# Kernel optimization log

Measured on AMD Instinct MI355X. Metric: run time of the kernel, lower is better.

Reference implementation:

```python
import jax, jax.numpy as jnp
import numpy as np

EPS = 1e-5  # torch LayerNorm default

def _ln(x, g, b):
    m = jnp.mean(x, axis=-1, keepdims=True)
    v = jnp.var(x, axis=-1, keepdims=True)
    return (x - m) / jnp.sqrt(v + EPS) * g + b

def setup_inputs() -> dict:
    B, S, F, H = 32, 512, 32, 128
    key = jax.random.key(0)
    ks = jax.random.split(key, 20)
    sc = 0.05
    inp = {
        "x": jax.random.normal(ks[0], (B, S, F), dtype=jnp.float32),
        # per-feature GRNs, stacked along F. fc1: Linear(1,H) -> weight vec (F,H)
        "fw1": jax.random.normal(ks[1], (F, H), dtype=jnp.float32) * sc,
        "fb1": jax.random.normal(ks[2], (F, H), dtype=jnp.float32) * sc,
        "fw2": jax.random.normal(ks[3], (F, H, H), dtype=jnp.float32) * sc,
        "fb2": jax.random.normal(ks[4], (F, H), dtype=jnp.float32) * sc,
        "fglu_w": jax.random.normal(ks[5], (F, H, 2 * H), dtype=jnp.float32) * sc,
        "fglu_b": jax.random.normal(ks[6], (F, 2 * H), dtype=jnp.float32) * sc,
        "fskip": jax.random.normal(ks[7], (F, H), dtype=jnp.float32) * sc,  # skip_proj Linear(1,H,bias=False)
        "fln_g": jnp.ones((F, H), dtype=jnp.float32),
        "fln_b": jnp.zeros((F, H), dtype=jnp.float32),
        # weight GRN: Linear(F,H)->ELU->Linear(H,F)->GLU(F)->LN(F); skip is identity (F==F)
        "ww1": jax.random.normal(ks[8], (F, H), dtype=jnp.float32) * sc,
        "wb1": jax.random.normal(ks[9], (H,), dtype=jnp.float32) * sc,
        "ww2": jax.random.normal(ks[10], (H, F), dtype=jnp.float32) * sc,
        "wb2": jax.random.normal(ks[11], (F,), dtype=jnp.float32) * sc,
        "wglu_w": jax.random.normal(ks[12], (F, 2 * F), dtype=jnp.float32) * sc,
        "wglu_b": jax.random.normal(ks[13], (2 * F,), dtype=jnp.float32) * sc,
        "wln_g": jnp.ones((F,), dtype=jnp.float32),
        "wln_b": jnp.zeros((F,), dtype=jnp.float32),
    }
    return inp

def reference(x, fw1, fb1, fw2, fb2, fglu_w, fglu_b, fskip, fln_g, fln_b,
              ww1, wb1, ww2, wb2, wglu_w, wglu_b, wln_g, wln_b):
    # ---- per-feature GRNs, batched over the F axis (dropout = eval, identity) ----
    # fc1(Linear(1,H)) + ELU : x[...,f] is a scalar per token
    h = jax.nn.elu(x[..., None] * fw1 + fb1)                 # (B,S,F,H)
    h = jnp.einsum('bsfh,fho->bsfo', h, fw2) + fb2           # fc2 (B,S,F,H)
    g = jnp.einsum('bsfh,fho->bsfo', h, fglu_w) + fglu_b     # GLU pre-act (B,S,F,2H)
    v, gate = jnp.split(g, 2, axis=-1)
    glu = v * jax.nn.sigmoid(gate)                           # (B,S,F,H)
    skip = x[..., None] * fskip                              # skip_proj (B,S,F,H)
    processed = _ln(glu + skip, fln_g[None, None], fln_b[None, None])  # (B,S,F,H)

    # ---- weight GRN over the full feature vector ----
    wh = jax.nn.elu(jnp.einsum('bsf,fh->bsh', x, ww1) + wb1)  # (B,S,H)
    wh = jnp.einsum('bsh,hf->bsf', wh, ww2) + wb2             # (B,S,F)
    wg = jnp.einsum('bsf,fg->bsg', wh, wglu_w) + wglu_b       # (B,S,2F)
    wv, wgate = jnp.split(wg, 2, axis=-1)
    wglu = wv * jax.nn.sigmoid(wgate)
    w = _ln(wglu + x, wln_g, wln_b)                           # skip is identity (F==F)
    weights = jax.nn.softmax(w, axis=-1)                      # (B,S,F)

    out = jnp.einsum('bsf,bsfh->bsh', weights, processed)     # weighted combine
    return (out, weights)
```

## Files before the change

kernel.cpp:

```cpp
#include <hip/hip_runtime.h>
#include <cstdint>
#include <cstddef>

#define NTOK 16384
#define FDIM 32
#define HDIM 128
#define TOKB 32

typedef __attribute__((ext_vector_type(8))) short short8;
typedef __attribute__((ext_vector_type(4))) float float4v;
typedef __attribute__((ext_vector_type(2))) float float2v;
typedef __attribute__((ext_vector_type(4))) unsigned int uint4v;

__device__ __forceinline__ float elu_f(float x)  { return x > 0.f ? x : __expf(x) - 1.f; }
__device__ __forceinline__ float sigm_f(float x) { return 1.f / (1.f + __expf(-x)); }

__device__ __forceinline__ unsigned int f2bf(float f) {
  unsigned int u = __float_as_uint(f);
  u += 0x7FFFu + ((u >> 16) & 1u);
  return u >> 16;
}
__device__ __forceinline__ unsigned int cvtpk(float lo, float hi) {
  unsigned int r;
  asm("v_cvt_pk_bf16_f32 %0, %1, %2" : "=v"(r) : "v"(lo), "v"(hi));
  return r;
}

__global__ __launch_bounds__(256) void k_pw(
    const float* __restrict__ x,
    const float* __restrict__ fw2, const float* __restrict__ fb2,
    const float* __restrict__ fglu_w, const float* __restrict__ fglu_b,
    const float* __restrict__ ww1, const float* __restrict__ wb1,
    const float* __restrict__ ww2, const float* __restrict__ wb2,
    const float* __restrict__ wglu_w, const float* __restrict__ wglu_b,
    const float* __restrict__ wln_g, const float* __restrict__ wln_b,
    unsigned short* __restrict__ bfrag, float* __restrict__ bcomb,
    float* __restrict__ wout)
{
  __shared__ __align__(16) float smem[4096];
  const int tid = threadIdx.x;

  if (blockIdx.x < 128) {
    const int f  = blockIdx.x >> 2;
    const int ks = blockIdx.x & 3;
    const float* src = fw2 + ((size_t)f * 128 + ks * 32) * 128;
    for (int i = 0; i < 4; ++i) {
      int vi = tid + i * 256;
      *(float4v*)&smem[vi * 4] = *(const float4v*)&src[vi * 4];
    }
    __syncthreads();

    const int o2 = tid;
    float acc[32];
#pragma unroll
    for (int kk = 0; kk < 32; ++kk) acc[kk] = 0.f;
    float bacc = 0.f;

    for (int o = 0; o < 128; o += 4) {
      float gv0 = fglu_w[((size_t)f * 128 + o + 0) * 256 + o2];
      float gv1 = fglu_w[((size_t)f * 128 + o + 1) * 256 + o2];
      float gv2 = fglu_w[((size_t)f * 128 + o + 2) * 256 + o2];
      float gv3 = fglu_w[((size_t)f * 128 + o + 3) * 256 + o2];
      bacc += fb2[f * 128 + o + 0] * gv0 + fb2[f * 128 + o + 1] * gv1
            + fb2[f * 128 + o + 2] * gv2 + fb2[f * 128 + o + 3] * gv3;
#pragma unroll
      for (int kk = 0; kk < 32; ++kk) {
        float4v a4 = *(const float4v*)&smem[kk * 128 + o];
        acc[kk] += a4[0] * gv0 + a4[1] * gv1 + a4[2] * gv2 + a4[3] * gv3;
      }
    }

    const int type = o2 >> 7;
    const int h    = o2 & 127;
    const int w2   = h >> 4;
    const int r    = h & 15;
    const size_t tbase = ((((size_t)f * 8 + w2) * 2 + type) * 4 + ks) * 512;
#pragma unroll
    for (int gg = 0; gg < 4; ++gg) {
      uint4v pk;
      pk[0] = f2bf(acc[gg * 8 + 0]) | (f2bf(acc[gg * 8 + 1]) << 16);
      pk[1] = f2bf(acc[gg * 8 + 2]) | (f2bf(acc[gg * 8 + 3]) << 16);
      pk[2] = f2bf(acc[gg * 8 + 4]) | (f2bf(acc[gg * 8 + 5]) << 16);
      pk[3] = f2bf(acc[gg * 8 + 6]) | (f2bf(acc[gg * 8 + 7]) << 16);
      *(uint4v*)(bfrag + tbase + (size_t)(r + gg * 16) * 8) = pk;
    }
    if (ks == 0)
      bcomb[f * 256 + o2] = bacc + fglu_b[f * 256 + o2];

  } else {
    const int bid = blockIdx.x - 128;
    const int wv  = tid >> 6;
    const int l   = tid & 63;
    const int t   = bid * 4 + wv;
    float* S = smem + wv * 256;

    float xv = x[(size_t)t * 32 + (l & 31)];
    if (l < 32) S[l] = xv;
    float a0 = wb1[l], a1 = wb1[l + 64];
    __syncthreads();
    for (int f2 = 0; f2 < 32; ++f2) {
      float xf = S[f2];
      a0 = fmaf(xf, ww1[f2 * 128 + l], a0);
      a1 = fmaf(xf, ww1[f2 * 128 + l + 64], a1);
    }
    a0 = elu_f(a0); a1 = elu_f(a1);
    S[32 + l] = a0; S[32 + l + 64] = a1;
    __syncthreads();

    const int o    = l & 31;
    const int half = l >> 5;
    float b = 0.f;
    for (int hh = 0; hh < 64; ++hh)
      b = fmaf(S[32 + half * 64 + hh], ww2[(half * 64 + hh) * 32 + o], b);
    b += __shfl_xor(b, 32);
    b += wb2[o];
    S[160 + o] = b;
    __syncthreads();

    float g = wglu_b[l];
    for (int o2i = 0; o2i < 32; ++o2i)
      g = fmaf(S[160 + o2i], wglu_w[o2i * 64 + l], g);

    float gate = __shfl_xor(g, 32);
    float y = g * sigm_f(gate) + xv;
    float s = y;
    s += __shfl_xor(s, 1); s += __shfl_xor(s, 2); s += __shfl_xor(s, 4);
    s += __shfl_xor(s, 8); s += __shfl_xor(s, 16);
    float mean = s * (1.f / 32.f);
    float d = y - mean;
    float ss = d * d;
    ss += __shfl_xor(ss, 1); ss += __shfl_xor(ss, 2); ss += __shfl_xor(ss, 4);
    ss += __shfl_xor(ss, 8); ss += __shfl_xor(ss, 16);
    float rstd = rsqrtf(ss * (1.f / 32.f) + 1e-5f);
    const int cc = l & 31;
    float ln = d * rstd * wln_g[cc] + wln_b[cc];
    float mx = ln;
    mx = fmaxf(mx, __shfl_xor(mx, 1));  mx = fmaxf(mx, __shfl_xor(mx, 2));
    mx = fmaxf(mx, __shfl_xor(mx, 4));  mx = fmaxf(mx, __shfl_xor(mx, 8));
    mx = fmaxf(mx, __shfl_xor(mx, 16));
    float e = __expf(ln - mx);
    float se = e;
    se += __shfl_xor(se, 1); se += __shfl_xor(se, 2); se += __shfl_xor(se, 4);
    se += __shfl_xor(se, 8); se += __shfl_xor(se, 16);
    if (l < 32) wout[(size_t)t * 32 + l] = e / se;
  }
}

__global__ __launch_bounds__(512, 4) void k_main(
    const float* __restrict__ x,
    const float* __restrict__ fw1, const float* __restrict__ fb1,
    const float* __restrict__ fskip, const float* __restrict__ flng,
    const float* __restrict__ flnb,
    const unsigned short* __restrict__ bfrag, const float* __restrict__ bcomb,
    const float* __restrict__ wts, float* __restrict__ out)
{
  __shared__ __align__(16) unsigned short a_lds[TOKB * 128];
  __shared__ __align__(16) float x_lds[FDIM * TOKB];
  __shared__ __align__(16) float w_lds[FDIM * TOKB];
  __shared__ __align__(16) float sred[2][2][TOKB];

  const int tid = threadIdx.x;
  const int w   = tid >> 6;
  const int l   = tid & 63;
  const int tk  = l & 15;
  const int rg  = l >> 4;
  const int t0  = blockIdx.x * TOKB;
  const int h0  = w * 16 + rg * 4;

  {
    float2v xv = *(const float2v*)(x   + (size_t)t0 * FDIM + tid * 2);
    float2v wv = *(const float2v*)(wts + (size_t)t0 * FDIM + tid * 2);
#pragma unroll
    for (int e = 0; e < 2; ++e) {
      int flat = tid * 2 + e;
      int tt = flat >> 5, ff = flat & 31;
      x_lds[ff * TOKB + tt] = xv[e];
      w_lds[ff * TOKB + tt] = wv[e];
    }
    if (tid < 64) ((float*)sred)[tid] = 0.f;
  }

  float4v oa0 = (float4v){0.f, 0.f, 0.f, 0.f};
  float4v oa1 = (float4v){0.f, 0.f, 0.f, 0.f};

  __syncthreads();

#pragma unroll 1
  for (int f = 0; f < FDIM; ++f) {
    {
      int st = tid >> 4;
      int sk = (tid & 15) * 8;
      float xf = x_lds[f * TOKB + st];
      float4v w1a = *(const float4v*)(fw1 + f * HDIM + sk);
      float4v w1b = *(const float4v*)(fw1 + f * HDIM + sk + 4);
      float4v b1a = *(const float4v*)(fb1 + f * HDIM + sk);
      float4v b1b = *(const float4v*)(fb1 + f * HDIM + sk + 4);
      uint4v pk;
      pk[0] = cvtpk(elu_f(fmaf(xf, w1a[0], b1a[0])),
                    elu_f(fmaf(xf, w1a[1], b1a[1])));
      pk[1] = cvtpk(elu_f(fmaf(xf, w1a[2], b1a[2])),
                    elu_f(fmaf(xf, w1a[3], b1a[3])));
      pk[2] = cvtpk(elu_f(fmaf(xf, w1b[0], b1b[0])),
                    elu_f(fmaf(xf, w1b[1], b1b[1])));
      pk[3] = cvtpk(elu_f(fmaf(xf, w1b[2], b1b[2])),
                    elu_f(fmaf(xf, w1b[3], b1b[3])));
      int sb = st * 256 + sk * 2;
      sb ^= (st & 7) << 4;
      *(uint4v*)((char*)a_lds + sb) = pk;
    }

    short8 aV[4], aG[4];
    {
      const unsigned short* bb = bfrag + (((size_t)f * 8 + w) * 8) * 512 + (size_t)l * 8;
#pragma unroll
      for (int ks = 0; ks < 4; ++ks) {
        aV[ks] = *(const short8*)(bb + (size_t)ks * 512);
        aG[ks] = *(const short8*)(bb + (size_t)(4 + ks) * 512);
      }
    }
    float4v bcv = *(const float4v*)(bcomb + f * 256 + h0);
    float4v bcg = *(const float4v*)(bcomb + f * 256 + 128 + h0);
    float4v fs4 = *(const float4v*)(fskip + f * HDIM + h0);
    float4v lg4 = *(const float4v*)(flng  + f * HDIM + h0);
    float4v lb4 = *(const float4v*)(flnb  + f * HDIM + h0);
    float xt0 = x_lds[f * TOKB + tk],      wt0 = w_lds[f * TOKB + tk];
    float xt1 = x_lds[f * TOKB + 16 + tk], wt1 = w_lds[f * TOKB + 16 + tk];

    __syncthreads();

    float4v av0 = (float4v){0.f,0.f,0.f,0.f}, ag0 = av0, av1 = av0, ag1 = av0;
#pragma unroll
    for (int ks = 0; ks < 4; ++ks) {
      int b0 = tk * 256 + (ks * 32 + rg * 8) * 2;
      b0 ^= (tk & 7) << 4;
      short8 hf0 = *(const short8*)((const char*)a_lds + b0);
      int b1 = (16 + tk) * 256 + (ks * 32 + rg * 8) * 2;
      b1 ^= (tk & 7) << 4;
      short8 hf1 = *(const short8*)((const char*)a_lds + b1);
      av0 = __builtin_amdgcn_mfma_f32_16x16x32_bf16(aV[ks], hf0, av0, 0, 0, 0);
      ag0 = __builtin_amdgcn_mfma_f32_16x16x32_bf16(aG[ks], hf0, ag0, 0, 0, 0);
      av1 = __builtin_amdgcn_mfma_f32_16x16x32_bf16(aV[ks], hf1, av1, 0, 0, 0);
      ag1 = __builtin_amdgcn_mfma_f32_16x16x32_bf16(aG[ks], hf1, ag1, 0, 0, 0);
    }

    const int cb = f & 1, nb = cb ^ 1;
    float4v y0, y1;
    float s0 = 0.f, ss0 = 0.f, s1 = 0.f, ss1 = 0.f;
#pragma unroll
    for (int i = 0; i < 4; ++i) {
      float ya = fmaf(xt0, fs4[i], (av0[i] + bcv[i]) * sigm_f(ag0[i] + bcg[i]));
      float yb = fmaf(xt1, fs4[i], (av1[i] + bcv[i]) * sigm_f(ag1[i] + bcg[i]));
      y0[i] = ya; y1[i] = yb;
      s0 += ya; ss0 = fmaf(ya, ya, ss0);
      s1 += yb; ss1 = fmaf(yb, yb, ss1);
    }
    s0  += __shfl_xor(s0, 16);  s0  += __shfl_xor(s0, 32);
    ss0 += __shfl_xor(ss0, 16); ss0 += __shfl_xor(ss0, 32);
    s1  += __shfl_xor(s1, 16);  s1  += __shfl_xor(s1, 32);
    ss1 += __shfl_xor(ss1, 16); ss1 += __shfl_xor(ss1, 32);
    if (rg == 0) {
      atomicAdd(&sred[cb][0][tk], s0);
      atomicAdd(&sred[cb][0][16 + tk], s1);
    } else if (rg == 1) {
      atomicAdd(&sred[cb][1][tk], ss0);
      atomicAdd(&sred[cb][1][16 + tk], ss1);
    }
    if (tid < 64) ((float*)(sred[nb]))[tid] = 0.f;

    __syncthreads();

    {
      float sA  = sred[cb][0][tk],      ssA = sred[cb][1][tk];
      float sB  = sred[cb][0][16 + tk], ssB = sred[cb][1][16 + tk];
      float m0 = sA * (1.f / 128.f);
      float m1 = sB * (1.f / 128.f);
      float v0 = fmaf(-m0, m0, ssA * (1.f / 128.f));
      float v1 = fmaf(-m1, m1, ssB * (1.f / 128.f));
      float rw0 = rsqrtf(v0 + 1e-5f) * wt0;
      float rw1 = rsqrtf(v1 + 1e-5f) * wt1;
#pragma unroll
      for (int i = 0; i < 4; ++i) {
        oa0[i] = fmaf((y0[i] - m0) * rw0, lg4[i], fmaf(wt0, lb4[i], oa0[i]));
        oa1[i] = fmaf((y1[i] - m1) * rw1, lg4[i], fmaf(wt1, lb4[i], oa1[i]));
      }
    }
  }

  *(float4v*)(out + (size_t)(t0 + tk) * HDIM + h0)      = oa0;
  *(float4v*)(out + (size_t)(t0 + 16 + tk) * HDIM + h0) = oa1;
}

extern "C" void kernel_launch(void* const* d_in, const int* in_sizes, int n_in,
                              void* d_out, int out_size, void* d_ws, size_t ws_size,
                              hipStream_t stream) {
  const float* x      = (const float*)d_in[0];
  const float* fw1    = (const float*)d_in[1];
  const float* fb1    = (const float*)d_in[2];
  const float* fw2    = (const float*)d_in[3];
  const float* fb2    = (const float*)d_in[4];
  const float* fglu_w = (const float*)d_in[5];
  const float* fglu_b = (const float*)d_in[6];
  const float* fskip  = (const float*)d_in[7];
  const float* fln_g  = (const float*)d_in[8];
  const float* fln_b  = (const float*)d_in[9];
  const float* ww1    = (const float*)d_in[10];
  const float* wb1    = (const float*)d_in[11];
  const float* ww2    = (const float*)d_in[12];
  const float* wb2    = (const float*)d_in[13];
  const float* wglu_w = (const float*)d_in[14];
  const float* wglu_b = (const float*)d_in[15];
  const float* wln_g  = (const float*)d_in[16];
  const float* wln_b  = (const float*)d_in[17];

  float* outp = (float*)d_out;
  float* wout = outp + (size_t)NTOK * HDIM;

  unsigned short* bfrag = (unsigned short*)d_ws;
  float* bcomb = (float*)((char*)d_ws + (size_t)2 * 1024 * 1024);

  k_pw<<<dim3(128 + NTOK / 4), dim3(256), 0, stream>>>(
      x, fw2, fb2, fglu_w, fglu_b, ww1, wb1, ww2, wb2,
      wglu_w, wglu_b, wln_g, wln_b, bfrag, bcomb, wout);
  k_main<<<dim3(NTOK / TOKB), dim3(512), 0, stream>>>(
      x, fw1, fb1, fskip, fln_g, fln_b, bfrag, bcomb, wout, outp);
}
```

Baseline: 156.5 us.

## Double-buffer weight fragments across features and pack per-feature scalars contiguously

The main loop is unrolled by two with ping-pong register buffers, so the bf16 MFMA weight fragments for feature f+1 are loaded from global memory while feature f is being computed. The fragment layout is changed so each lane reads one contiguous 128-byte run instead of eight strided chunks. The GLU biases, skip weights and LayerNorm gamma/beta are packed into one per-feature scalar block to cut separate load streams. The cost is higher register pressure from two fragment sets under a launch bound of 4, which could cause spills or lower occupancy.

Result: slower. 367.5 us (+134.8%).

```diff
diff --git a/kernel.cpp b/kernel.cpp
--- a/kernel.cpp
+++ b/kernel.cpp
@@ -30,11 +30,13 @@
     const float* __restrict__ x,
     const float* __restrict__ fw2, const float* __restrict__ fb2,
     const float* __restrict__ fglu_w, const float* __restrict__ fglu_b,
+    const float* __restrict__ fskip, const float* __restrict__ flng,
+    const float* __restrict__ flnb,
     const float* __restrict__ ww1, const float* __restrict__ wb1,
     const float* __restrict__ ww2, const float* __restrict__ wb2,
     const float* __restrict__ wglu_w, const float* __restrict__ wglu_b,
     const float* __restrict__ wln_g, const float* __restrict__ wln_b,
-    unsigned short* __restrict__ bfrag, float* __restrict__ bcomb,
+    unsigned short* __restrict__ bfrag, float* __restrict__ scal,
     float* __restrict__ wout)
 {
   __shared__ __align__(16) float smem[4096];
@@ -74,7 +76,6 @@
     const int h    = o2 & 127;
     const int w2   = h >> 4;
     const int r    = h & 15;
-    const size_t tbase = ((((size_t)f * 8 + w2) * 2 + type) * 4 + ks) * 512;
 #pragma unroll
     for (int gg = 0; gg < 4; ++gg) {
       uint4v pk;
@@ -82,10 +83,18 @@
       pk[1] = f2bf(acc[gg * 8 + 2]) | (f2bf(acc[gg * 8 + 3]) << 16);
       pk[2] = f2bf(acc[gg * 8 + 4]) | (f2bf(acc[gg * 8 + 5]) << 16);
       pk[3] = f2bf(acc[gg * 8 + 6]) | (f2bf(acc[gg * 8 + 7]) << 16);
-      *(uint4v*)(bfrag + tbase + (size_t)(r + gg * 16) * 8) = pk;
-    }
-    if (ks == 0)
-      bcomb[f * 256 + o2] = bacc + fglu_b[f * 256 + o2];
+      size_t off = ((((size_t)f * 8 + w2) * 64 + (r + gg * 16)) * 8
+                    + (type * 4 + ks)) * 8;
+      *(uint4v*)(bfrag + off) = pk;
+    }
+    if (ks == 0) {
+      scal[f * 640 + type * 128 + h] = bacc + fglu_b[f * 256 + o2];
+      if (type == 0) {
+        scal[f * 640 + 256 + h] = fskip[f * 128 + h];
+        scal[f * 640 + 384 + h] = flng[f * 128 + h];
+        scal[f * 640 + 512 + h] = flnb[f * 128 + h];
+      }
+    }
 
   } else {
     const int bid = blockIdx.x - 128;
@@ -146,12 +155,104 @@
   }
 }
 
+#define FBODY(F, AVc, AGc, AVn, AGn) {                                        \
+                                  \
+    {                                                                         \
+      float xf = x_lds[(F) * TOKB + st];                                      \
+      float4v w1a = *(const float4v*)(fw1 + (F) * HDIM + sk);                 \
+      float4v w1b = *(const float4v*)(fw1 + (F) * HDIM + sk + 4);             \
+      float4v b1a = *(const float4v*)(fb1 + (F) * HDIM + sk);                 \
+      float4v b1b = *(const float4v*)(fb1 + (F) * HDIM + sk + 4);             \
+      uint4v pk;                                                              \
+      pk[0] = cvtpk(elu_f(fmaf(xf, w1a[0], b1a[0])),                          \
+                    elu_f(fmaf(xf, w1a[1], b1a[1])));                         \
+      pk[1] = cvtpk(elu_f(fmaf(xf, w1a[2], b1a[2])),                          \
+                    elu_f(fmaf(xf, w1a[3], b1a[3])));                         \
+      pk[2] = cvtpk(elu_f(fmaf(xf, w1b[0], b1b[0])),                          \
+                    elu_f(fmaf(xf, w1b[1], b1b[1])));                         \
+      pk[3] = cvtpk(elu_f(fmaf(xf, w1b[2], b1b[2])),                          \
+                    elu_f(fmaf(xf, w1b[3], b1b[3])));                         \
+      *(uint4v*)((char*)a_lds + stg_byte) = pk;                               \
+    }                                                                         \
+                               \
+    const float* sp = scal + (size_t)(F) * 640 + h0;                          \
+    float4v bcv = *(const float4v*)(sp);                                      \
+    float4v bcg = *(const float4v*)(sp + 128);                                \
+    float4v fs4 = *(const float4v*)(sp + 256);                                \
+    float4v lg4 = *(const float4v*)(sp + 384);                                \
+    float4v lb4 = *(const float4v*)(sp + 512);                                \
+    float xt0 = x_lds[(F) * TOKB + tk],      wt0 = w_lds[(F) * TOKB + tk];    \
+    float xt1 = x_lds[(F) * TOKB + 16 + tk], wt1 = w_lds[(F) * TOKB + 16 + tk];\
+              \
+    if ((F) + 1 < FDIM) {                                                     \
+      const unsigned short* nb_ =                                             \
+          bfrag + ((((size_t)(F) + 1) * 8 + w) * 64 + l) * 64;                \
+      _Pragma("unroll")                                                       \
+      for (int ks = 0; ks < 4; ++ks) {                                        \
+        AVn[ks] = *(const short8*)(nb_ + ks * 8);                             \
+        AGn[ks] = *(const short8*)(nb_ + 32 + ks * 8);                        \
+      }                                                                       \
+    }                                                                         \
+    __syncthreads();                                     \
+    float4v av0 = (float4v){0.f,0.f,0.f,0.f}, ag0 = av0, av1 = av0, ag1 = av0;\
+    _Pragma("unroll")                                                         \
+    for (int ks = 0; ks < 4; ++ks) {                                          \
+      int b0 = tk * 256 + (ks * 32 + rg * 8) * 2;                             \
+      b0 ^= (tk & 7) << 4;                                                    \
+      short8 hf0 = *(const short8*)((const char*)a_lds + b0);                 \
+      int b1 = (16 + tk) * 256 + (ks * 32 + rg * 8) * 2;                      \
+      b1 ^= (tk & 7) << 4;                                                    \
+      short8 hf1 = *(const short8*)((const char*)a_lds + b1);                 \
+      av0 = __builtin_amdgcn_mfma_f32_16x16x32_bf16(AVc[ks], hf0, av0, 0,0,0);\
+      ag0 = __builtin_amdgcn_mfma_f32_16x16x32_bf16(AGc[ks], hf0, ag0, 0,0,0);\
+      av1 = __builtin_amdgcn_mfma_f32_16x16x32_bf16(AVc[ks], hf1, av1, 0,0,0);\
+      ag1 = __builtin_amdgcn_mfma_f32_16x16x32_bf16(AGc[ks], hf1, ag1, 0,0,0);\
+    }                                                                         \
+    const int cb = (F) & 1, nb2 = cb ^ 1;                                     \
+    float4v y0, y1;                                                           \
+    float s0 = 0.f, ss0 = 0.f, s1 = 0.f, ss1 = 0.f;                           \
+    _Pragma("unroll")                                                         \
+    for (int i = 0; i < 4; ++i) {                                             \
+      float ya = fmaf(xt0, fs4[i], (av0[i] + bcv[i]) * sigm_f(ag0[i] + bcg[i]));\
+      float yb = fmaf(xt1, fs4[i], (av1[i] + bcv[i]) * sigm_f(ag1[i] + bcg[i]));\
+      y0[i] = ya; y1[i] = yb;                                                 \
+      s0 += ya; ss0 = fmaf(ya, ya, ss0);                                      \
+      s1 += yb; ss1 = fmaf(yb, yb, ss1);                                      \
+    }                                                                         \
+    s0  += __shfl_xor(s0, 16);  s0  += __shfl_xor(s0, 32);                    \
+    ss0 += __shfl_xor(ss0, 16); ss0 += __shfl_xor(ss0, 32);                   \
+    s1  += __shfl_xor(s1, 16);  s1  += __shfl_xor(s1, 32);                    \
+    ss1 += __shfl_xor(ss1, 16); ss1 += __shfl_xor(ss1, 32);                   \
+    if (rg == 0) {                                                            \
+      atomicAdd(&sred[cb][0][tk], s0);                                        \
+      atomicAdd(&sred[cb][0][16 + tk], s1);                                   \
+    } else if (rg == 1) {                                                     \
+      atomicAdd(&sred[cb][1][tk], ss0);                                       \
+      atomicAdd(&sred[cb][1][16 + tk], ss1);                                  \
+    }                                                                         \
+    if (tid < 64) ((float*)(sred[nb2]))[tid] = 0.f;                           \
+    __syncthreads();                               \
+    {                                                                         \
+      float sA  = sred[cb][0][tk],      ssA = sred[cb][1][tk];                \
+      float sB  = sred[cb][0][16 + tk], ssB = sred[cb][1][16 + tk];           \
+      float m0 = sA * (1.f / 128.f);                                          \
+      float m1 = sB * (1.f / 128.f);                                          \
+      float v0 = fmaf(-m0, m0, ssA * (1.f / 128.f));                          \
+      float v1 = fmaf(-m1, m1, ssB * (1.f / 128.f));                          \
+      float rw0 = rsqrtf(v0 + 1e-5f) * wt0;                                   \
+      float rw1 = rsqrtf(v1 + 1e-5f) * wt1;                                   \
+      _Pragma("unroll")                                                       \
+      for (int i = 0; i < 4; ++i) {                                           \
+        oa0[i] = fmaf((y0[i] - m0) * rw0, lg4[i], fmaf(wt0, lb4[i], oa0[i])); \
+        oa1[i] = fmaf((y1[i] - m1) * rw1, lg4[i], fmaf(wt1, lb4[i], oa1[i])); \
+      }                                                                       \
+    }                                                                         \
+  }
+
 __global__ __launch_bounds__(512, 4) void k_main(
     const float* __restrict__ x,
     const float* __restrict__ fw1, const float* __restrict__ fb1,
-    const float* __restrict__ fskip, const float* __restrict__ flng,
-    const float* __restrict__ flnb,
-    const unsigned short* __restrict__ bfrag, const float* __restrict__ bcomb,
+    const unsigned short* __restrict__ bfrag, const float* __restrict__ scal,
     const float* __restrict__ wts, float* __restrict__ out)
 {
   __shared__ __align__(16) unsigned short a_lds[TOKB * 128];
@@ -166,6 +267,9 @@
   const int rg  = l >> 4;
   const int t0  = blockIdx.x * TOKB;
   const int h0  = w * 16 + rg * 4;
+  const int st  = tid >> 4;
+  const int sk  = (tid & 15) * 8;
+  const int stg_byte = (st * 256 + sk * 2) ^ ((st & 7) << 4);
 
   {
     float2v xv = *(const float2v*)(x   + (size_t)t0 * FDIM + tid * 2);
@@ -183,107 +287,21 @@
   float4v oa0 = (float4v){0.f, 0.f, 0.f, 0.f};
   float4v oa1 = (float4v){0.f, 0.f, 0.f, 0.f};
 
+  short8 aVA[4], aGA[4], aVB[4], aGB[4];
+  {
+    const unsigned short* bb = bfrag + ((size_t)w * 64 + l) * 64;
+#pragma unroll
+    for (int ks = 0; ks < 4; ++ks) {
+      aVA[ks] = *(const short8*)(bb + ks * 8);
+      aGA[ks] = *(const short8*)(bb + 32 + ks * 8);
+    }
+  }
+
   __syncthreads();
 
-#pragma unroll 1
-  for (int f = 0; f < FDIM; ++f) {
-    {
-      int st = tid >> 4;
-      int sk = (tid & 15) * 8;
-      float xf = x_lds[f * TOKB + st];
-      float4v w1a = *(const float4v*)(fw1 + f * HDIM + sk);
-      float4v w1b = *(const float4v*)(fw1 + f * HDIM + sk + 4);
-      float4v b1a = *(const float4v*)(fb1 + f * HDIM + sk);
-      float4v b1b = *(const float4v*)(fb1 + f * HDIM + sk + 4);
-      uint4v pk;
-      pk[0] = cvtpk(elu_f(fmaf(xf, w1a[0], b1a[0])),
-                    elu_f(fmaf(xf, w1a[1], b1a[1])));
-      pk[1] = cvtpk(elu_f(fmaf(xf, w1a[2], b1a[2])),
-                    elu_f(fmaf(xf, w1a[3], b1a[3])));
-      pk[2] = cvtpk(elu_f(fmaf(xf, w1b[0], b1b[0])),
-                    elu_f(fmaf(xf, w1b[1], b1b[1])));
-      pk[3] = cvtpk(elu_f(fmaf(xf, w1b[2], b1b[2])),
-                    elu_f(fmaf(xf, w1b[3], b1b[3])));
-      int sb = st * 256 + sk * 2;
-      sb ^= (st & 7) << 4;
-      *(uint4v*)((char*)a_lds + sb) = pk;
-    }
-
-    short8 aV[4], aG[4];
-    {
-      const unsigned short* bb = bfrag + (((size_t)f * 8 + w) * 8) * 512 + (size_t)l * 8;
-#pragma unroll
-      for (int ks = 0; ks < 4; ++ks) {
-        aV[ks] = *(const short8*)(bb + (size_t)ks * 512);
-        aG[ks] = *(const short8*)(bb + (size_t)(4 + ks) * 512);
-      }
-    }
-    float4v bcv = *(const float4v*)(bcomb + f * 256 + h0);
-    float4v bcg = *(const float4v*)(bcomb + f * 256 + 128 + h0);
-    float4v fs4 = *(const float4v*)(fskip + f * HDIM + h0);
-    float4v lg4 = *(const float4v*)(flng  + f * HDIM + h0);
-    float4v lb4 = *(const float4v*)(flnb  + f * HDIM + h0);
-    float xt0 = x_lds[f * TOKB + tk],      wt0 = w_lds[f * TOKB + tk];
-    float xt1 = x_lds[f * TOKB + 16 + tk], wt1 = w_lds[f * TOKB + 16 + tk];
-
-    __syncthreads();
-
-    float4v av0 = (float4v){0.f,0.f,0.f,0.f}, ag0 = av0, av1 = av0, ag1 = av0;
-#pragma unroll
-    for (int ks = 0; ks < 4; ++ks) {
-      int b0 = tk * 256 + (ks * 32 + rg * 8) * 2;
-      b0 ^= (tk & 7) << 4;
-      short8 hf0 = *(const short8*)((const char*)a_lds + b0);
-      int b1 = (16 + tk) * 256 + (ks * 32 + rg * 8) * 2;
-      b1 ^= (tk & 7) << 4;
-      short8 hf1 = *(const short8*)((const char*)a_lds + b1);
-      av0 = __builtin_amdgcn_mfma_f32_16x16x32_bf16(aV[ks], hf0, av0, 0, 0, 0);
-      ag0 = __builtin_amdgcn_mfma_f32_16x16x32_bf16(aG[ks], hf0, ag0, 0, 0, 0);
-      av1 = __builtin_amdgcn_mfma_f32_16x16x32_bf16(aV[ks], hf1, av1, 0, 0, 0);
-      ag1 = __builtin_amdgcn_mfma_f32_16x16x32_bf16(aG[ks], hf1, ag1, 0, 0, 0);
-    }
-
-    const int cb = f & 1, nb = cb ^ 1;
-    float4v y0, y1;
-    float s0 = 0.f, ss0 = 0.f, s1 = 0.f, ss1 = 0.f;
-#pragma unroll
-    for (int i = 0; i < 4; ++i) {
-      float ya = fmaf(xt0, fs4[i], (av0[i] + bcv[i]) * sigm_f(ag0[i] + bcg[i]));
-      float yb = fmaf(xt1, fs4[i], (av1[i] + bcv[i]) * sigm_f(ag1[i] + bcg[i]));
-      y0[i] = ya; y1[i] = yb;
-      s0 += ya; ss0 = fmaf(ya, ya, ss0);
-      s1 += yb; ss1 = fmaf(yb, yb, ss1);
-    }
-    s0  += __shfl_xor(s0, 16);  s0  += __shfl_xor(s0, 32);
-    ss0 += __shfl_xor(ss0, 16); ss0 += __shfl_xor(ss0, 32);
-    s1  += __shfl_xor(s1, 16);  s1  += __shfl_xor(s1, 32);
-    ss1 += __shfl_xor(ss1, 16); ss1 += __shfl_xor(ss1, 32);
-    if (rg == 0) {
-      atomicAdd(&sred[cb][0][tk], s0);
-      atomicAdd(&sred[cb][0][16 + tk], s1);
-    } else if (rg == 1) {
-      atomicAdd(&sred[cb][1][tk], ss0);
-      atomicAdd(&sred[cb][1][16 + tk], ss1);
-    }
-    if (tid < 64) ((float*)(sred[nb]))[tid] = 0.f;
-
-    __syncthreads();
-
-    {
-      float sA  = sred[cb][0][tk],      ssA = sred[cb][1][tk];
-      float sB  = sred[cb][0][16 + tk], ssB = sred[cb][1][16 + tk];
-      float m0 = sA * (1.f / 128.f);
-      float m1 = sB * (1.f / 128.f);
-      float v0 = fmaf(-m0, m0, ssA * (1.f / 128.f));
-      float v1 = fmaf(-m1, m1, ssB * (1.f / 128.f));
-      float rw0 = rsqrtf(v0 + 1e-5f) * wt0;
-      float rw1 = rsqrtf(v1 + 1e-5f) * wt1;
-#pragma unroll
-      for (int i = 0; i < 4; ++i) {
-        oa0[i] = fmaf((y0[i] - m0) * rw0, lg4[i], fmaf(wt0, lb4[i], oa0[i]));
-        oa1[i] = fmaf((y1[i] - m1) * rw1, lg4[i], fmaf(wt1, lb4[i], oa1[i]));
-      }
-    }
+  for (int f = 0; f < FDIM; f += 2) {
+    FBODY(f,     aVA, aGA, aVB, aGB);
+    FBODY(f + 1, aVB, aGB, aVA, aGA);
   }
 
   *(float4v*)(out + (size_t)(t0 + tk) * HDIM + h0)      = oa0;
@@ -316,11 +334,12 @@
   float* wout = outp + (size_t)NTOK * HDIM;
 
   unsigned short* bfrag = (unsigned short*)d_ws;
-  float* bcomb = (float*)((char*)d_ws + (size_t)2 * 1024 * 1024);
+  float* scal = (float*)((char*)d_ws + (size_t)2 * 1024 * 1024);
 
   k_pw<<<dim3(128 + NTOK / 4), dim3(256), 0, stream>>>(
-      x, fw2, fb2, fglu_w, fglu_b, ww1, wb1, ww2, wb2,
-      wglu_w, wglu_b, wln_g, wln_b, bfrag, bcomb, wout);
+      x, fw2, fb2, fglu_w, fglu_b, fskip, fln_g, fln_b,
+      ww1, wb1, ww2, wb2, wglu_w, wglu_b, wln_g, wln_b,
+      bfrag, scal, wout);
   k_main<<<dim3(NTOK / TOKB), dim3(512), 0, stream>>>(
-      x, fw1, fb1, fskip, fln_g, fln_b, bfrag, bcomb, wout, outp);
-}
+      x, fw1, fb1, bfrag, scal, wout, outp);
+}
```

## Pipeline LayerNorm finalize one iteration behind to drop a barrier per feature

Applied to the files above, without the earlier changes.

The main loop used two __syncthreads per feature: one after staging the ELU activations and one after the LayerNorm stat atomics. Now the A tile is double-buffered and the stats use a triple-buffered reduction array. The normalize-and-accumulate for feature f-1 is deferred into iteration f after the single barrier, which removes one block barrier per feature. Per-feature scalars (GLU bias, skip, LN gamma/beta) are also packed into one contiguous workspace array by the prep kernel, which merges several scattered loads. In exchange the kernel keeps more live registers (previous y, gamma, beta, weights) and uses more LDS, which may lower occupancy.

New measurement: 143.7 us. -8.2%, faster.

```diff
diff --git a/kernel.cpp b/kernel.cpp
--- a/kernel.cpp
+++ b/kernel.cpp
@@ -30,11 +30,13 @@
     const float* __restrict__ x,
     const float* __restrict__ fw2, const float* __restrict__ fb2,
     const float* __restrict__ fglu_w, const float* __restrict__ fglu_b,
+    const float* __restrict__ fskip, const float* __restrict__ flng,
+    const float* __restrict__ flnb,
     const float* __restrict__ ww1, const float* __restrict__ wb1,
     const float* __restrict__ ww2, const float* __restrict__ wb2,
     const float* __restrict__ wglu_w, const float* __restrict__ wglu_b,
     const float* __restrict__ wln_g, const float* __restrict__ wln_b,
-    unsigned short* __restrict__ bfrag, float* __restrict__ bcomb,
+    unsigned short* __restrict__ bfrag, float* __restrict__ scal,
     float* __restrict__ wout)
 {
   __shared__ __align__(16) float smem[4096];
@@ -84,8 +86,14 @@
       pk[3] = f2bf(acc[gg * 8 + 6]) | (f2bf(acc[gg * 8 + 7]) << 16);
       *(uint4v*)(bfrag + tbase + (size_t)(r + gg * 16) * 8) = pk;
     }
-    if (ks == 0)
-      bcomb[f * 256 + o2] = bacc + fglu_b[f * 256 + o2];
+    if (ks == 0) {
+      scal[f * 640 + type * 128 + h] = bacc + fglu_b[f * 256 + o2];
+      if (type == 0) {
+        scal[f * 640 + 256 + h] = fskip[f * 128 + h];
+        scal[f * 640 + 384 + h] = flng[f * 128 + h];
+        scal[f * 640 + 512 + h] = flnb[f * 128 + h];
+      }
+    }
 
   } else {
     const int bid = blockIdx.x - 128;
@@ -149,15 +157,13 @@
 __global__ __launch_bounds__(512, 4) void k_main(
     const float* __restrict__ x,
     const float* __restrict__ fw1, const float* __restrict__ fb1,
-    const float* __restrict__ fskip, const float* __restrict__ flng,
-    const float* __restrict__ flnb,
-    const unsigned short* __restrict__ bfrag, const float* __restrict__ bcomb,
+    const unsigned short* __restrict__ bfrag, const float* __restrict__ scal,
     const float* __restrict__ wts, float* __restrict__ out)
 {
-  __shared__ __align__(16) unsigned short a_lds[TOKB * 128];
+  __shared__ __align__(16) unsigned short a_lds[2][TOKB * 128];
   __shared__ __align__(16) float x_lds[FDIM * TOKB];
   __shared__ __align__(16) float w_lds[FDIM * TOKB];
-  __shared__ __align__(16) float sred[2][2][TOKB];
+  __shared__ __align__(16) float sred[3][2][TOKB];
 
   const int tid = threadIdx.x;
   const int w   = tid >> 6;
@@ -166,6 +172,9 @@
   const int rg  = l >> 4;
   const int t0  = blockIdx.x * TOKB;
   const int h0  = w * 16 + rg * 4;
+  const int st  = tid >> 4;
+  const int sk  = (tid & 15) * 8;
+  const int stg_byte = (st * 256 + sk * 2) ^ ((st & 7) << 4);
 
   {
     float2v xv = *(const float2v*)(x   + (size_t)t0 * FDIM + tid * 2);
@@ -177,19 +186,38 @@
       x_lds[ff * TOKB + tt] = xv[e];
       w_lds[ff * TOKB + tt] = wv[e];
     }
-    if (tid < 64) ((float*)sred)[tid] = 0.f;
+    if (tid < 192) ((float*)sred)[tid] = 0.f;
   }
 
   float4v oa0 = (float4v){0.f, 0.f, 0.f, 0.f};
   float4v oa1 = (float4v){0.f, 0.f, 0.f, 0.f};
+  float4v py0, py1, plg, plb;
+  float pwt0 = 0.f, pwt1 = 0.f;
 
   __syncthreads();
 
+  int cb = 0;
 #pragma unroll 1
   for (int f = 0; f < FDIM; ++f) {
+    short8 aV[4], aG[4];
     {
-      int st = tid >> 4;
-      int sk = (tid & 15) * 8;
+      const unsigned short* bb = bfrag + (((size_t)f * 8 + w) * 8) * 512 + (size_t)l * 8;
+#pragma unroll
+      for (int ks = 0; ks < 4; ++ks) {
+        aV[ks] = *(const short8*)(bb + (size_t)ks * 512);
+        aG[ks] = *(const short8*)(bb + (size_t)(4 + ks) * 512);
+      }
+    }
+    const float* sp = scal + (size_t)f * 640 + h0;
+    float4v bcv = *(const float4v*)(sp);
+    float4v bcg = *(const float4v*)(sp + 128);
+    float4v fs4 = *(const float4v*)(sp + 256);
+    float4v lg4 = *(const float4v*)(sp + 384);
+    float4v lb4 = *(const float4v*)(sp + 512);
+    float xt0 = x_lds[f * TOKB + tk],      wt0 = w_lds[f * TOKB + tk];
+    float xt1 = x_lds[f * TOKB + 16 + tk], wt1 = w_lds[f * TOKB + 16 + tk];
+
+    {
       float xf = x_lds[f * TOKB + st];
       float4v w1a = *(const float4v*)(fw1 + f * HDIM + sk);
       float4v w1b = *(const float4v*)(fw1 + f * HDIM + sk + 4);
@@ -204,27 +232,8 @@
                     elu_f(fmaf(xf, w1b[1], b1b[1])));
       pk[3] = cvtpk(elu_f(fmaf(xf, w1b[2], b1b[2])),
                     elu_f(fmaf(xf, w1b[3], b1b[3])));
-      int sb = st * 256 + sk * 2;
-      sb ^= (st & 7) << 4;
-      *(uint4v*)((char*)a_lds + sb) = pk;
-    }
-
-    short8 aV[4], aG[4];
-    {
-      const unsigned short* bb = bfrag + (((size_t)f * 8 + w) * 8) * 512 + (size_t)l * 8;
-#pragma unroll
-      for (int ks = 0; ks < 4; ++ks) {
-        aV[ks] = *(const short8*)(bb + (size_t)ks * 512);
-        aG[ks] = *(const short8*)(bb + (size_t)(4 + ks) * 512);
-      }
-    }
-    float4v bcv = *(const float4v*)(bcomb + f * 256 + h0);
-    float4v bcg = *(const float4v*)(bcomb + f * 256 + 128 + h0);
-    float4v fs4 = *(const float4v*)(fskip + f * HDIM + h0);
-    float4v lg4 = *(const float4v*)(flng  + f * HDIM + h0);
-    float4v lb4 = *(const float4v*)(flnb  + f * HDIM + h0);
-    float xt0 = x_lds[f * TOKB + tk],      wt0 = w_lds[f * TOKB + tk];
-    float xt1 = x_lds[f * TOKB + 16 + tk], wt1 = w_lds[f * TOKB + 16 + tk];
+      *(uint4v*)((char*)a_lds[f & 1] + stg_byte) = pk;
+    }
 
     __syncthreads();
 
@@ -233,24 +242,39 @@
     for (int ks = 0; ks < 4; ++ks) {
       int b0 = tk * 256 + (ks * 32 + rg * 8) * 2;
       b0 ^= (tk & 7) << 4;
-      short8 hf0 = *(const short8*)((const char*)a_lds + b0);
+      short8 hf0 = *(const short8*)((const char*)a_lds[f & 1] + b0);
       int b1 = (16 + tk) * 256 + (ks * 32 + rg * 8) * 2;
       b1 ^= (tk & 7) << 4;
-      short8 hf1 = *(const short8*)((const char*)a_lds + b1);
+      short8 hf1 = *(const short8*)((const char*)a_lds[f & 1] + b1);
       av0 = __builtin_amdgcn_mfma_f32_16x16x32_bf16(aV[ks], hf0, av0, 0, 0, 0);
       ag0 = __builtin_amdgcn_mfma_f32_16x16x32_bf16(aG[ks], hf0, ag0, 0, 0, 0);
       av1 = __builtin_amdgcn_mfma_f32_16x16x32_bf16(aV[ks], hf1, av1, 0, 0, 0);
       ag1 = __builtin_amdgcn_mfma_f32_16x16x32_bf16(aG[ks], hf1, ag1, 0, 0, 0);
     }
 
-    const int cb = f & 1, nb = cb ^ 1;
-    float4v y0, y1;
+    if (f > 0) {
+      const int pb = (cb == 0) ? 2 : cb - 1;
+      float sA  = sred[pb][0][tk],      ssA = sred[pb][1][tk];
+      float sB  = sred[pb][0][16 + tk], ssB = sred[pb][1][16 + tk];
+      float m0 = sA * (1.f / 128.f);
+      float m1 = sB * (1.f / 128.f);
+      float v0 = fmaf(-m0, m0, ssA * (1.f / 128.f));
+      float v1 = fmaf(-m1, m1, ssB * (1.f / 128.f));
+      float rw0 = rsqrtf(v0 + 1e-5f) * pwt0;
+      float rw1 = rsqrtf(v1 + 1e-5f) * pwt1;
+#pragma unroll
+      for (int i = 0; i < 4; ++i) {
+        oa0[i] = fmaf((py0[i] - m0) * rw0, plg[i], fmaf(pwt0, plb[i], oa0[i]));
+        oa1[i] = fmaf((py1[i] - m1) * rw1, plg[i], fmaf(pwt1, plb[i], oa1[i]));
+      }
+    }
+
     float s0 = 0.f, ss0 = 0.f, s1 = 0.f, ss1 = 0.f;
 #pragma unroll
     for (int i = 0; i < 4; ++i) {
       float ya = fmaf(xt0, fs4[i], (av0[i] + bcv[i]) * sigm_f(ag0[i] + bcg[i]));
       float yb = fmaf(xt1, fs4[i], (av1[i] + bcv[i]) * sigm_f(ag1[i] + bcg[i]));
-      y0[i] = ya; y1[i] = yb;
+      py0[i] = ya; py1[i] = yb;
       s0 += ya; ss0 = fmaf(ya, ya, ss0);
       s1 += yb; ss1 = fmaf(yb, yb, ss1);
     }
@@ -265,24 +289,30 @@
       atomicAdd(&sred[cb][1][tk], ss0);
       atomicAdd(&sred[cb][1][16 + tk], ss1);
     }
-    if (tid < 64) ((float*)(sred[nb]))[tid] = 0.f;
-
-    __syncthreads();
-
     {
-      float sA  = sred[cb][0][tk],      ssA = sred[cb][1][tk];
-      float sB  = sred[cb][0][16 + tk], ssB = sred[cb][1][16 + tk];
-      float m0 = sA * (1.f / 128.f);
-      float m1 = sB * (1.f / 128.f);
-      float v0 = fmaf(-m0, m0, ssA * (1.f / 128.f));
-      float v1 = fmaf(-m1, m1, ssB * (1.f / 128.f));
-      float rw0 = rsqrtf(v0 + 1e-5f) * wt0;
-      float rw1 = rsqrtf(v1 + 1e-5f) * wt1;
-#pragma unroll
-      for (int i = 0; i < 4; ++i) {
-        oa0[i] = fmaf((y0[i] - m0) * rw0, lg4[i], fmaf(wt0, lb4[i], oa0[i]));
-        oa1[i] = fmaf((y1[i] - m1) * rw1, lg4[i], fmaf(wt1, lb4[i], oa1[i]));
-      }
+      const int nb = (cb == 2) ? 0 : cb + 1;
+      if (tid < 64) ((float*)(sred[nb]))[tid] = 0.f;
+    }
+
+    pwt0 = wt0; pwt1 = wt1; plg = lg4; plb = lb4;
+    cb = (cb == 2) ? 0 : cb + 1;
+  }
+
+  __syncthreads();
+  {
+    const int pb = (cb == 0) ? 2 : cb - 1;
+    float sA  = sred[pb][0][tk],      ssA = sred[pb][1][tk];
+    float sB  = sred[pb][0][16 + tk], ssB = sred[pb][1][16 + tk];
+    float m0 = sA * (1.f / 128.f);
+    float m1 = sB * (1.f / 128.f);
+    float v0 = fmaf(-m0, m0, ssA * (1.f / 128.f));
+    float v1 = fmaf(-m1, m1, ssB * (1.f / 128.f));
+    float rw0 = rsqrtf(v0 + 1e-5f) * pwt0;
+    float rw1 = rsqrtf(v1 + 1e-5f) * pwt1;
+#pragma unroll
+    for (int i = 0; i < 4; ++i) {
+      oa0[i] = fmaf((py0[i] - m0) * rw0, plg[i], fmaf(pwt0, plb[i], oa0[i]));
+      oa1[i] = fmaf((py1[i] - m1) * rw1, plg[i], fmaf(pwt1, plb[i], oa1[i]));
     }
   }
 
@@ -316,11 +346,12 @@
   float* wout = outp + (size_t)NTOK * HDIM;
 
   unsigned short* bfrag = (unsigned short*)d_ws;
-  float* bcomb = (float*)((char*)d_ws + (size_t)2 * 1024 * 1024);
+  float* scal = (float*)((char*)d_ws + (size_t)2 * 1024 * 1024);
 
   k_pw<<<dim3(128 + NTOK / 4), dim3(256), 0, stream>>>(
-      x, fw2, fb2, fglu_w, fglu_b, ww1, wb1, ww2, wb2,
-      wglu_w, wglu_b, wln_g, wln_b, bfrag, bcomb, wout);
+      x, fw2, fb2, fglu_w, fglu_b, fskip, fln_g, fln_b,
+      ww1, wb1, ww2, wb2, wglu_w, wglu_b, wln_g, wln_b,
+      bfrag, scal, wout);
   k_main<<<dim3(NTOK / TOKB), dim3(512), 0, stream>>>(
-      x, fw1, fb1, fskip, fln_g, fln_b, bfrag, bcomb, wout, outp);
-}
+      x, fw1, fb1, bfrag, scal, wout, outp);
+}
```
